# Kernel tuning notes

Measured on AMD Instinct MI355X. Metric: run time of the kernel, lower is better.

The kernel has to match this reference:

```python
import jax, jax.numpy as jnp
import numpy as np

N = 50000      # nodes
E = 800000     # edges (avg degree 16)
NF = 128       # input feature dim
H = 128        # hidden dim
GAMMA = 1.0    # gm init arg
COS_EPS = 1e-8 # F.cosine_similarity eps
EW_MIN = 1e-4  # edge-weight clamp


def setup_inputs() -> dict:
    key = jax.random.key(0)
    ks = jax.random.split(key, 9)
    x = jax.random.normal(ks[0], (N, NF), dtype=jnp.float32)
    edge_index = jax.random.randint(ks[1], (2, E), 0, N, dtype=jnp.int64)
    sensitive_attr = jax.random.randint(ks[2], (N,), 0, 2, dtype=jnp.int64)
    s1 = 1.0 / np.sqrt(NF)
    s2 = 1.0 / np.sqrt(H)
    W1 = jax.random.normal(ks[3], (NF, H), dtype=jnp.float32) * s1
    b1 = jnp.zeros((H,), dtype=jnp.float32)
    W2 = jax.random.normal(ks[4], (H, H), dtype=jnp.float32) * s2
    b2 = jnp.zeros((H,), dtype=jnp.float32)
    Wc = jax.random.normal(ks[5], (H, 1), dtype=jnp.float32) * s2
    bc = jnp.zeros((1,), dtype=jnp.float32)
    return {"x": x, "edge_index": edge_index, "sensitive_attr": sensitive_attr,
            "W1": W1, "b1": b1, "W2": W2, "b2": b2, "Wc": Wc, "bc": bc}


def gcn_conv(x, W, b, src, dst, ew, n):
    """PyG GCNConv: lin -> symmetric-normalized edge-weighted aggregation (+self loops) -> bias."""
    xt = x @ W                                              # [N,H]
    deg = jax.ops.segment_sum(ew, dst, num_segments=n) + 1.0  # self-loop weight 1
    dinv = jnp.where(deg > 0, deg ** -0.5, 0.0)             # [N]
    norm = dinv[src] * ew * dinv[dst]                       # [E]
    agg = jax.ops.segment_sum(xt[src] * norm[:, None], dst, num_segments=n)
    # self-loop contribution: norm_ii = dinv[i] * 1 * dinv[i]
    return agg + xt * (dinv * dinv)[:, None] + b


def reference(x, edge_index, sensitive_attr, W1, b1, W2, b2, Wc, bc):
    src, dst = edge_index[0], edge_index[1]
    # cosine-similarity edge weights (gather-heavy)
    xs, xd = x[src], x[dst]                                  # [E,F] each
    dot = jnp.sum(xs * xd, axis=1)
    ns = jnp.maximum(jnp.sqrt(jnp.sum(xs * xs, axis=1)), COS_EPS)
    nd = jnp.maximum(jnp.sqrt(jnp.sum(xd * xd, axis=1)), COS_EPS)
    sim = dot / (ns * nd)
    sen_diff = (sensitive_attr[src] != sensitive_attr[dst]).astype(x.dtype)
    ew = jnp.maximum(sim * jnp.exp(-GAMMA * sen_diff), EW_MIN)
    # two GCN layers (dropout is identity in eval mode)
    h = jax.nn.relu(gcn_conv(x, W1, b1, src, dst, ew, N))
    h = jax.nn.relu(gcn_conv(h, W2, b2, src, dst, ew, N))
    y = h @ Wc + bc                                          # [N,1]
    return (y, h)
```

## Files before the change

### kernel.cpp

```cpp
#include <hip/hip_runtime.h>


typedef unsigned short u16;
typedef unsigned int u32;
typedef __attribute__((ext_vector_type(8))) short short8;
typedef __attribute__((ext_vector_type(4))) float floatx4;

__device__ __forceinline__ float bflo(u32 u){ return __uint_as_float(u << 16); }
__device__ __forceinline__ float bfhi(u32 u){ return __uint_as_float(u & 0xFFFF0000u); }
__device__ __forceinline__ float bf1(u16 u){ return __uint_as_float(((u32)u) << 16); }
__device__ __forceinline__ u16 f2bf(float f){
    u32 u = __float_as_uint(f);
    u += 0x7FFFu + ((u >> 16) & 1u);
    return (u16)(u >> 16);
}
__device__ __forceinline__ u32 pack2(float a, float b){
    return (u32)f2bf(a) | ((u32)f2bf(b) << 16);
}
__device__ __forceinline__ float wsum(float v){
#pragma unroll
    for (int o = 32; o > 0; o >>= 1) v += __shfl_xor(v, o, 64);
    return v;
}
__device__ __forceinline__ float ld1(const void* p, size_t idx, int f32){
    return f32 ? ((const float*)p)[idx] : bf1(((const u16*)p)[idx]);
}
__device__ __forceinline__ int ldidx(const int* p, size_t i, int i64){
    return i64 ? p[2 * i] : p[i];
}

__global__ void classify_k(const u32* __restrict__ xw, const int* __restrict__ eiw,
                           int* __restrict__ flags, int* __restrict__ bcnt)
{
    __shared__ int c_out, c_nz;
    int t = threadIdx.x;
    if (t == 0) { c_out = 0; c_nz = 0; }
    if (t < 256) bcnt[t] = 0;
    __syncthreads();
    u32 w = xw[t];
    int e = (w >> 7) & 0xFF;
    int outl = (e < 110 || e > 140) ? 1 : 0;
    int nz = (eiw[2 * t + 1] != 0) ? 1 : 0;
    atomicAdd(&c_out, outl);
    atomicAdd(&c_nz, nz);
    __syncthreads();
    if (t == 0) { flags[0] = (c_out > 256); flags[1] = (c_nz < 256); }
}

__global__ __launch_bounds__(256) void convhist_k(const void* __restrict__ x,
                                                  u32* __restrict__ xb,
                                                  float* __restrict__ rn, int N,
                                                  const int* __restrict__ ei,
                                                  const int* __restrict__ sa,
                                                  int* __restrict__ bcnt, int E,
                                                  const void* __restrict__ W1,
                                                  const void* __restrict__ W2,
                                                  uint4* __restrict__ wf1,
                                                  uint4* __restrict__ wf2,
                                                  const int* __restrict__ flags,
                                                  int nbN, int nbH)
{
    __shared__ int lb[256];
    int b = blockIdx.x;
    if (b < nbN) {
        int i = b * 4 + (threadIdx.x >> 6);
        if (i >= N) return;
        int lane = threadIdx.x & 63;
        u32 u;
        if (flags[0]) {
            const float* q = (const float*)x + (size_t)i * 128 + lane * 2;
            u = pack2(q[0], q[1]);
        } else u = ((const u32*)x)[(size_t)i * 64 + lane];
        xb[(size_t)i * 64 + lane] = u;
        float f0 = bflo(u), f1 = bfhi(u);
        float ss = wsum(f0 * f0 + f1 * f1);
        if (lane == 0) {
            float r = 1.0f / fmaxf(sqrtf(ss), 1e-8f);
            int a = flags[1] ? sa[2 * (size_t)i] : sa[i];
            rn[i] = a ? -r : r;
        }
    } else if (b < nbN + nbH) {
        int t = threadIdx.x;
        lb[t] = 0;
        __syncthreads();
        int i64 = flags[1];
        size_t base = (size_t)(b - nbN) * 8192;
#pragma unroll 4
        for (int k = 0; k < 32; ++k) {
            size_t e = base + (size_t)k * 256 + t;
            if (e < (size_t)E) {
                int d = ldidx(ei, (size_t)E + e, i64);
                if ((u32)d >= (u32)N) d = 0;
                atomicAdd(&lb[d >> 8], 1);
            }
        }
        __syncthreads();
        int c = lb[t];
        if (c) atomicAdd(&bcnt[t], c);
    } else {
        int slot = (b - nbN - nbH) * 256 + threadIdx.x;
        if (slot >= 4096) return;
        int f32w = flags[0];
        const void* W = (slot < 2048) ? W1 : W2;
        uint4* wf = (slot < 2048) ? wf1 : wf2;
        int s = slot & 2047;
        int lane = s & 63, kk = (s >> 6) & 3, ct = s >> 8;
        int q = lane >> 4, n = lane & 15;
        int col = ct * 16 + n, k0 = kk * 32 + q * 8;
        union { u16 us[8]; uint4 u4; } tmp;
#pragma unroll
        for (int j = 0; j < 8; ++j)
            tmp.us[j] = f2bf(ld1(W, (size_t)(k0 + j) * 128 + col, f32w));
        wf[s] = tmp.u4;
    }
}

__global__ void bscan_k(const int* __restrict__ bcnt, int* __restrict__ bbase,
                        int* __restrict__ bcur, int* __restrict__ rowp, int N)
{
    int lane = threadIdx.x;
    int carry = 0;
    for (int base = 0; base < 256; base += 64) {
        int i = base + lane;
        int v = bcnt[i];
        int sc = v;
#pragma unroll
        for (int o = 1; o < 64; o <<= 1) {
            int nv = __shfl_up(sc, o);
            if (lane >= o) sc += nv;
        }
        int excl = carry + sc - v;
        bbase[i] = excl;
        bcur[i] = excl;
        carry += __shfl(sc, 63);
    }
    if (lane == 0) { bbase[256] = carry; rowp[N] = carry; }
}

__global__ __launch_bounds__(256) void bucket_k(const int* __restrict__ ei,
                                                int* __restrict__ bcur,
                                                u32* __restrict__ tmp,
                                                int E, int N,
                                                const int* __restrict__ flags)
{
    __shared__ int lh[256];
    __shared__ int gb[256];
    int t = threadIdx.x;
    lh[t] = 0;
    __syncthreads();
    int i64 = flags[1];
    size_t base = (size_t)blockIdx.x * 4096;
    u32 pay[16], meta[16];
#pragma unroll
    for (int k = 0; k < 16; ++k) {
        size_t e = base + (size_t)k * 256 + t;
        if (e < (size_t)E) {
            int s = ldidx(ei, e, i64);
            int d = ldidx(ei, (size_t)E + e, i64);
            if ((u32)s >= (u32)N) s = 0;
            if ((u32)d >= (u32)N) d = 0;
            int b = d >> 8;
            pay[k] = ((u32)s << 8) | ((u32)d & 0xFFu);
            int r = atomicAdd(&lh[b], 1);
            meta[k] = ((u32)r << 8) | (u32)b;
        } else meta[k] = 0xFFFFFFFFu;
    }
    __syncthreads();
    int c = lh[t];
    gb[t] = c ? atomicAdd(&bcur[t], c) : 0;
    __syncthreads();
#pragma unroll
    for (int k = 0; k < 16; ++k) {
        if (meta[k] != 0xFFFFFFFFu) {
            int b = (int)(meta[k] & 0xFFu);
            int r = (int)(meta[k] >> 8);
            tmp[gb[b] + r] = pay[k];
        }
    }
}

__global__ __launch_bounds__(256) void scat2_k(const int* __restrict__ bbase,
                                               int* __restrict__ rowp,
                                               const u32* __restrict__ tmp,
                                               u32* __restrict__ rec,
                                               int N, int E)
{
    __shared__ int lcnt[256];
    __shared__ int wtot[4];
    int b = blockIdx.x, t = threadIdx.x;
    int lane = t & 63, w = t >> 6;
    int n0 = b << 8;
    int p0 = bbase[b], p1 = bbase[b + 1];
    if (p0 < 0) p0 = 0;
    if (p1 > E) p1 = E;
    lcnt[t] = 0;
    __syncthreads();
    for (int idx = p0 + t; idx < p1; idx += 256)
        atomicAdd(&lcnt[tmp[idx] & 0xFFu], 1);
    __syncthreads();
    int v = lcnt[t];
    int sc = v;
#pragma unroll
    for (int o = 1; o < 64; o <<= 1) {
        int nv = __shfl_up(sc, o);
        if (lane >= o) sc += nv;
    }
    if (lane == 63) wtot[w] = sc;
    __syncthreads();
    int wo = 0;
#pragma unroll
    for (int k = 0; k < 4; ++k) { int s = wtot[k]; if (k < w) wo += s; }
    int excl = wo + sc - v;
    int node = n0 + t;
    if (node < N) rowp[node] = p0 + excl;
    lcnt[t] = excl;
    __syncthreads();
    for (int idx = p0 + t; idx < p1; idx += 256) {
        u32 pay = tmp[idx];
        int r = atomicAdd(&lcnt[pay & 0xFFu], 1);
        int pos = p0 + r;
        if ((u32)pos >= (u32)E) pos = 0;
        rec[pos] = pay >> 8;
    }
}

__global__ __launch_bounds__(256) void ewcsr_k(const u32* __restrict__ xb,
                                               const float* __restrict__ rn,
                                               const int* __restrict__ rowp,
                                               u32* __restrict__ rec,
                                               float* __restrict__ dv,
                                               int N, int E)
{
    int i = blockIdx.x * 4 + (threadIdx.x >> 6);
    if (i >= N) return;
    int lane = threadIdx.x & 63, g = lane >> 4, j = lane & 15;
    uint4 D = ((const uint4*)(xb + (size_t)i * 64))[j];
    float rni = rn[i];
    int p0 = rowp[i], p1 = rowp[i + 1];
    if (p0 < 0) p0 = 0;
    if (p1 > E) p1 = E;
    float acc = 0.0f;
    int p = p0 + g;
    for (; p + 4 < p1; p += 8) {
        int s0 = (int)rec[p];     if ((u32)s0 >= (u32)N) s0 = 0;
        int s1 = (int)rec[p + 4]; if ((u32)s1 >= (u32)N) s1 = 0;
        uint4 A0 = ((const uint4*)(xb + (size_t)s0 * 64))[j];
        uint4 A1 = ((const uint4*)(xb + (size_t)s1 * 64))[j];
        float d0 = bflo(A0.x) * bflo(D.x) + bfhi(A0.x) * bfhi(D.x)
                 + bflo(A0.y) * bflo(D.y) + bfhi(A0.y) * bfhi(D.y)
                 + bflo(A0.z) * bflo(D.z) + bfhi(A0.z) * bfhi(D.z)
                 + bflo(A0.w) * bflo(D.w) + bfhi(A0.w) * bfhi(D.w);
        float d1 = bflo(A1.x) * bflo(D.x) + bfhi(A1.x) * bfhi(D.x)
                 + bflo(A1.y) * bflo(D.y) + bfhi(A1.y) * bfhi(D.y)
                 + bflo(A1.z) * bflo(D.z) + bfhi(A1.z) * bfhi(D.z)
                 + bflo(A1.w) * bflo(D.w) + bfhi(A1.w) * bfhi(D.w);
#pragma unroll
        for (int o = 8; o > 0; o >>= 1) {
            d0 += __shfl_xor(d0, o);
            d1 += __shfl_xor(d1, o);
        }
        if (j == 0) {
            float pr0 = rn[s0] * rni;
            float w0 = fmaxf(d0 * fabsf(pr0) *
                             ((pr0 < 0.0f) ? 0.36787944117144233f : 1.0f), 1e-4f);
            u16 wb0 = f2bf(w0);
            rec[p] = ((u32)s0 << 16) | wb0;
            acc += bf1(wb0);
            float pr1 = rn[s1] * rni;
            float w1 = fmaxf(d1 * fabsf(pr1) *
                             ((pr1 < 0.0f) ? 0.36787944117144233f : 1.0f), 1e-4f);
            u16 wb1 = f2bf(w1);
            rec[p + 4] = ((u32)s1 << 16) | wb1;
            acc += bf1(wb1);
        }
    }
    if (p < p1) {
        int s0 = (int)rec[p]; if ((u32)s0 >= (u32)N) s0 = 0;
        uint4 A0 = ((const uint4*)(xb + (size_t)s0 * 64))[j];
        float d0 = bflo(A0.x) * bflo(D.x) + bfhi(A0.x) * bfhi(D.x)
                 + bflo(A0.y) * bflo(D.y) + bfhi(A0.y) * bfhi(D.y)
                 + bflo(A0.z) * bflo(D.z) + bfhi(A0.z) * bfhi(D.z)
                 + bflo(A0.w) * bflo(D.w) + bfhi(A0.w) * bfhi(D.w);
#pragma unroll
        for (int o = 8; o > 0; o >>= 1) d0 += __shfl_xor(d0, o);
        if (j == 0) {
            float pr0 = rn[s0] * rni;
            float w0 = fmaxf(d0 * fabsf(pr0) *
                             ((pr0 < 0.0f) ? 0.36787944117144233f : 1.0f), 1e-4f);
            u16 wb0 = f2bf(w0);
            rec[p] = ((u32)s0 << 16) | wb0;
            acc += bf1(wb0);
        }
    }
    acc += __shfl_xor(acc, 16);
    acc += __shfl_xor(acc, 32);
    if (lane == 0) dv[i] = 1.0f / sqrtf(1.0f + acc);
}

__global__ __launch_bounds__(256) void agg_k(const u32* __restrict__ feat,
                                             const int* __restrict__ rowp,
                                             const u32* __restrict__ rec,
                                             const float* __restrict__ dinv,
                                             u32* __restrict__ Tb, int N, int E)
{
    int i = blockIdx.x * 4 + (threadIdx.x >> 6);
    if (i >= N) return;
    int lane = threadIdx.x & 63;
    float di = dinv[i], sc = di * di;
    u32 u = feat[(size_t)i * 64 + lane];
    float a0 = bflo(u) * sc, a1 = bfhi(u) * sc;
    int p0 = rowp[i], p1 = rowp[i + 1];
    if (p0 < 0) p0 = 0;
    if (p1 > E) p1 = E;
    int p = p0;
    for (; p + 7 < p1; p += 8) {
        u32 r[8]; int s[8]; u32 v[8];
#pragma unroll
        for (int k = 0; k < 8; ++k) {
            r[k] = rec[p + k];
            s[k] = r[k] >> 16;
            if (s[k] >= N) s[k] = 0;
        }
#pragma unroll
        for (int k = 0; k < 8; ++k) v[k] = feat[(size_t)s[k] * 64 + lane];
#pragma unroll
        for (int k = 0; k < 8; ++k) {
            float w = bf1((u16)r[k]) * di * dinv[s[k]];
            a0 = fmaf(w, bflo(v[k]), a0);
            a1 = fmaf(w, bfhi(v[k]), a1);
        }
    }
    for (; p + 1 < p1; p += 2) {
        u32 r0 = rec[p], r1 = rec[p + 1];
        int s0 = r0 >> 16, s1 = r1 >> 16;
        if (s0 >= N) s0 = 0;
        if (s1 >= N) s1 = 0;
        u32 v0 = feat[(size_t)s0 * 64 + lane];
        u32 v1 = feat[(size_t)s1 * 64 + lane];
        float w0 = bf1((u16)r0) * di * dinv[s0];
        float w1 = bf1((u16)r1) * di * dinv[s1];
        a0 = fmaf(w0, bflo(v0), a0); a1 = fmaf(w0, bfhi(v0), a1);
        a0 = fmaf(w1, bflo(v1), a0); a1 = fmaf(w1, bfhi(v1), a1);
    }
    if (p < p1) {
        u32 r0 = rec[p];
        int s0 = r0 >> 16;
        if (s0 >= N) s0 = 0;
        u32 v0 = feat[(size_t)s0 * 64 + lane];
        float w0 = bf1((u16)r0) * di * dinv[s0];
        a0 = fmaf(w0, bflo(v0), a0); a1 = fmaf(w0, bfhi(v0), a1);
    }
    Tb[(size_t)i * 64 + lane] = pack2(a0, a1);
}

__global__ __launch_bounds__(256) void gemm_m(const u32* __restrict__ Tb,
                                              const uint4* __restrict__ wfrag,
                                              const void* __restrict__ bias,
                                              void* __restrict__ out, int outbf,
                                              int N,
                                              const void* __restrict__ Wc,
                                              const void* __restrict__ bc,
                                              float* __restrict__ yout,
                                              const int* __restrict__ flags)
{
    int t = threadIdx.x, wave = t >> 6, lane = t & 63;
    int q = lane >> 4, n = lane & 15;
    int f32w = flags[0];
    int rowbase = blockIdx.x * 64 + wave * 16;
    int arow = rowbase + n; if (arow > N - 1) arow = N - 1;
    const uint4* ap = (const uint4*)(Tb + (size_t)arow * 64);
    short8 a[4];
#pragma unroll
    for (int kk = 0; kk < 4; ++kk) {
        uint4 av = ap[kk * 4 + q];
        a[kk] = *(short8*)&av;
    }
    floatx4 acc[8];
#pragma unroll
    for (int ct = 0; ct < 8; ++ct) acc[ct] = (floatx4){0.f, 0.f, 0.f, 0.f};
#pragma unroll
    for (int ct = 0; ct < 8; ++ct) {
#pragma unroll
        for (int kk = 0; kk < 4; ++kk) {
            uint4 bv = wfrag[(ct * 4 + kk) * 64 + lane];
            acc[ct] = __builtin_amdgcn_mfma_f32_16x16x32_bf16(
                a[kk], *(short8*)&bv, acc[ct], 0, 0, 0);
        }
    }
    float bcv = 0.0f;
    float part[4] = {0.f, 0.f, 0.f, 0.f};
    if (yout) bcv = ld1(bc, 0, f32w);
#pragma unroll
    for (int ct = 0; ct < 8; ++ct) {
        int col = ct * 16 + n;
        float bia = ld1(bias, col, f32w);
        float wcv = yout ? ld1(Wc, col, f32w) : 0.0f;
#pragma unroll
        for (int r = 0; r < 4; ++r) {
            int row = rowbase + q * 4 + r;
            float h = fmaxf(acc[ct][r] + bia, 0.0f);
            if (row < N) {
                if (outbf) ((u16*)out)[(size_t)row * 128 + col] = f2bf(h);
                else       ((float*)out)[(size_t)row * 128 + col] = h;
            }
            part[r] = fmaf(h, wcv, part[r]);
        }
    }
    if (yout) {
#pragma unroll
        for (int r = 0; r < 4; ++r) {
            float pr = part[r];
#pragma unroll
            for (int o = 8; o > 0; o >>= 1) pr += __shfl_xor(pr, o);
            int row = rowbase + q * 4 + r;
            if (n == 0 && row < N) yout[row] = pr + bcv;
        }
    }
}

extern "C" void kernel_launch(void* const* d_in, const int* in_sizes, int n_in,
                              void* d_out, int out_size, void* d_ws, size_t ws_size,
                              hipStream_t stream)
{
    const void* x  = d_in[0];
    const int* ei  = (const int*)d_in[1];
    const int* sa  = (const int*)d_in[2];
    const void* W1 = d_in[3];
    const void* b1 = d_in[4];
    const void* W2 = d_in[5];
    const void* b2 = d_in[6];
    const void* Wc = d_in[7];
    const void* bc = d_in[8];
    const int N = in_sizes[2];
    const int E = in_sizes[1] / 2;

    float* y_out = (float*)d_out;
    float* h_out = y_out + N;
    u32*   Tbuf  = (u32*)d_in[0];
    u32*   tmp   = (u32*)d_in[0];

    const int nbN = (N + 3) / 4;
    const int nbH = (E + 8191) / 8192;
    const int NB  = (N + 255) / 256;

    char* p = (char*)d_ws;
    auto carve = [&](size_t bytes) { char* r = p; p += (bytes + 255) & ~(size_t)255; return r; };
    int*   flags = (int*)carve(256);
    float* rn    = (float*)carve((size_t)N * 4);
    float* dinv  = (float*)carve((size_t)N * 4);
    int*   rowp  = (int*)carve((size_t)(N + 1) * 4);
    int*   bcnt  = (int*)carve(256 * 4);
    int*   bbase = (int*)carve(260 * 4);
    int*   bcur  = (int*)carve(256 * 4);
    uint4* wf1   = (uint4*)carve(2048 * 16);
    uint4* wf2   = (uint4*)carve(2048 * 16);
    u32*   rec   = (u32*)carve((size_t)E * 4);
    u32*   xb    = (u32*)carve((size_t)N * 64 * 4);

    classify_k<<<1, 1024, 0, stream>>>((const u32*)x, ei, flags, bcnt);
    convhist_k<<<nbN + nbH + 16, 256, 0, stream>>>(x, xb, rn, N, ei, sa, bcnt, E,
                                                   W1, W2, wf1, wf2, flags,
                                                   nbN, nbH);
    bscan_k<<<1, 64, 0, stream>>>(bcnt, bbase, bcur, rowp, N);
    bucket_k<<<(E + 4095) / 4096, 256, 0, stream>>>(ei, bcur, tmp, E, N, flags);
    scat2_k<<<NB, 256, 0, stream>>>(bbase, rowp, tmp, rec, N, E);
    ewcsr_k<<<(N + 3) / 4, 256, 0, stream>>>(xb, rn, rowp, rec, dinv, N, E);

    agg_k<<<(N + 3) / 4, 256, 0, stream>>>(xb, rowp, rec, dinv, Tbuf, N, E);
    gemm_m<<<(N + 63) / 64, 256, 0, stream>>>(Tbuf, wf1, b1, xb, 1, N,
                                              nullptr, nullptr, nullptr, flags);
    agg_k<<<(N + 3) / 4, 256, 0, stream>>>(xb, rowp, rec, dinv, Tbuf, N, E);
    gemm_m<<<(N + 63) / 64, 256, 0, stream>>>(Tbuf, wf2, b2, h_out, 0, N,
                                              Wc, bc, y_out, flags);
}
```

Before: 276.0 us.

## Fuse neighbor aggregation with MFMA GEMM via shared-memory tile

Merges the aggregation kernel and the MFMA GEMM kernel into one kernel per layer. Each wave aggregates 16 rows into a padded LDS tile, then the block runs the bf16 MFMA GEMM directly from LDS, so the intermediate aggregated buffer never goes through global memory and two launches are dropped. In exchange, each wave now walks 16 rows one after another and the block count falls by 16x (about 782 blocks), which lowers the number of gathers in flight and the parallelism available to hide their latency. Layer 1 output is written into a separate buffer (the x input region) that layer 2 reads.

```diff
diff --git a/kernel.cpp b/kernel.cpp
--- a/kernel.cpp
+++ b/kernel.cpp
@@ -297,82 +297,81 @@
     if (lane == 0) dv[i] = 1.0f / sqrtf(1.0f + acc);
 }
 
-__global__ __launch_bounds__(256) void agg_k(const u32* __restrict__ feat,
-                                             const int* __restrict__ rowp,
-                                             const u32* __restrict__ rec,
-                                             const float* __restrict__ dinv,
-                                             u32* __restrict__ Tb, int N, int E)
-{
-    int i = blockIdx.x * 4 + (threadIdx.x >> 6);
-    if (i >= N) return;
-    int lane = threadIdx.x & 63;
-    float di = dinv[i], sc = di * di;
-    u32 u = feat[(size_t)i * 64 + lane];
-    float a0 = bflo(u) * sc, a1 = bfhi(u) * sc;
-    int p0 = rowp[i], p1 = rowp[i + 1];
-    if (p0 < 0) p0 = 0;
-    if (p1 > E) p1 = E;
-    int p = p0;
-    for (; p + 7 < p1; p += 8) {
-        u32 r[8]; int s[8]; u32 v[8];
-#pragma unroll
-        for (int k = 0; k < 8; ++k) {
-            r[k] = rec[p + k];
-            s[k] = r[k] >> 16;
-            if (s[k] >= N) s[k] = 0;
-        }
-#pragma unroll
-        for (int k = 0; k < 8; ++k) v[k] = feat[(size_t)s[k] * 64 + lane];
-#pragma unroll
-        for (int k = 0; k < 8; ++k) {
-            float w = bf1((u16)r[k]) * di * dinv[s[k]];
-            a0 = fmaf(w, bflo(v[k]), a0);
-            a1 = fmaf(w, bfhi(v[k]), a1);
-        }
-    }
-    for (; p + 1 < p1; p += 2) {
-        u32 r0 = rec[p], r1 = rec[p + 1];
-        int s0 = r0 >> 16, s1 = r1 >> 16;
-        if (s0 >= N) s0 = 0;
-        if (s1 >= N) s1 = 0;
-        u32 v0 = feat[(size_t)s0 * 64 + lane];
-        u32 v1 = feat[(size_t)s1 * 64 + lane];
-        float w0 = bf1((u16)r0) * di * dinv[s0];
-        float w1 = bf1((u16)r1) * di * dinv[s1];
-        a0 = fmaf(w0, bflo(v0), a0); a1 = fmaf(w0, bfhi(v0), a1);
-        a0 = fmaf(w1, bflo(v1), a0); a1 = fmaf(w1, bfhi(v1), a1);
-    }
-    if (p < p1) {
-        u32 r0 = rec[p];
-        int s0 = r0 >> 16;
-        if (s0 >= N) s0 = 0;
-        u32 v0 = feat[(size_t)s0 * 64 + lane];
-        float w0 = bf1((u16)r0) * di * dinv[s0];
-        a0 = fmaf(w0, bflo(v0), a0); a1 = fmaf(w0, bfhi(v0), a1);
-    }
-    Tb[(size_t)i * 64 + lane] = pack2(a0, a1);
-}
-
-__global__ __launch_bounds__(256) void gemm_m(const u32* __restrict__ Tb,
-                                              const uint4* __restrict__ wfrag,
-                                              const void* __restrict__ bias,
-                                              void* __restrict__ out, int outbf,
-                                              int N,
-                                              const void* __restrict__ Wc,
-                                              const void* __restrict__ bc,
-                                              float* __restrict__ yout,
-                                              const int* __restrict__ flags)
-{
+__global__ __launch_bounds__(256) void aggemm_k(const u32* __restrict__ feat,
+                                                const int* __restrict__ rowp,
+                                                const u32* __restrict__ rec,
+                                                const float* __restrict__ dinv,
+                                                const uint4* __restrict__ wfrag,
+                                                const void* __restrict__ bias,
+                                                void* __restrict__ out, int outbf,
+                                                int N, int E,
+                                                const void* __restrict__ Wc,
+                                                const void* __restrict__ bc,
+                                                float* __restrict__ yout,
+                                                const int* __restrict__ flags)
+{
+    __shared__ u32 T[64 * 68];
     int t = threadIdx.x, wave = t >> 6, lane = t & 63;
+    int rowbase = blockIdx.x * 64 + wave * 16;
+    for (int r = 0; r < 16; ++r) {
+        int i = rowbase + r;
+        float a0 = 0.0f, a1 = 0.0f;
+        if (i < N) {
+            float di = dinv[i], sc = di * di;
+            u32 u = feat[(size_t)i * 64 + lane];
+            a0 = bflo(u) * sc; a1 = bfhi(u) * sc;
+            int p0 = rowp[i], p1 = rowp[i + 1];
+            if (p0 < 0) p0 = 0;
+            if (p1 > E) p1 = E;
+            int p = p0;
+            for (; p + 7 < p1; p += 8) {
+                u32 rr[8]; int s[8]; u32 v[8];
+#pragma unroll
+                for (int k = 0; k < 8; ++k) {
+                    rr[k] = rec[p + k];
+                    s[k] = rr[k] >> 16;
+                    if (s[k] >= N) s[k] = 0;
+                }
+#pragma unroll
+                for (int k = 0; k < 8; ++k) v[k] = feat[(size_t)s[k] * 64 + lane];
+#pragma unroll
+                for (int k = 0; k < 8; ++k) {
+                    float w = bf1((u16)rr[k]) * di * dinv[s[k]];
+                    a0 = fmaf(w, bflo(v[k]), a0);
+                    a1 = fmaf(w, bfhi(v[k]), a1);
+                }
+            }
+            for (; p + 1 < p1; p += 2) {
+                u32 r0 = rec[p], r1 = rec[p + 1];
+                int s0 = r0 >> 16, s1 = r1 >> 16;
+                if (s0 >= N) s0 = 0;
+                if (s1 >= N) s1 = 0;
+                u32 v0 = feat[(size_t)s0 * 64 + lane];
+                u32 v1 = feat[(size_t)s1 * 64 + lane];
+                float w0 = bf1((u16)r0) * di * dinv[s0];
+                float w1 = bf1((u16)r1) * di * dinv[s1];
+                a0 = fmaf(w0, bflo(v0), a0); a1 = fmaf(w0, bfhi(v0), a1);
+                a0 = fmaf(w1, bflo(v1), a0); a1 = fmaf(w1, bfhi(v1), a1);
+            }
+            if (p < p1) {
+                u32 r0 = rec[p];
+                int s0 = r0 >> 16;
+                if (s0 >= N) s0 = 0;
+                u32 v0 = feat[(size_t)s0 * 64 + lane];
+                float w0 = bf1((u16)r0) * di * dinv[s0];
+                a0 = fmaf(w0, bflo(v0), a0); a1 = fmaf(w0, bfhi(v0), a1);
+            }
+        }
+        T[(wave * 16 + r) * 68 + lane] = pack2(a0, a1);
+    }
+    __syncthreads();
     int q = lane >> 4, n = lane & 15;
     int f32w = flags[0];
-    int rowbase = blockIdx.x * 64 + wave * 16;
-    int arow = rowbase + n; if (arow > N - 1) arow = N - 1;
-    const uint4* ap = (const uint4*)(Tb + (size_t)arow * 64);
+    const u32* ap = T + (size_t)(wave * 16 + n) * 68;
     short8 a[4];
 #pragma unroll
     for (int kk = 0; kk < 4; ++kk) {
-        uint4 av = ap[kk * 4 + q];
+        uint4 av = *(const uint4*)(ap + (kk * 4 + q) * 4);
         a[kk] = *(short8*)&av;
     }
     floatx4 acc[8];
@@ -436,7 +435,7 @@
 
     float* y_out = (float*)d_out;
     float* h_out = y_out + N;
-    u32*   Tbuf  = (u32*)d_in[0];
+    u32*   h1b   = (u32*)d_in[0];
     u32*   tmp   = (u32*)d_in[0];
 
     const int nbN = (N + 3) / 4;
@@ -466,10 +465,10 @@
     scat2_k<<<NB, 256, 0, stream>>>(bbase, rowp, tmp, rec, N, E);
     ewcsr_k<<<(N + 3) / 4, 256, 0, stream>>>(xb, rn, rowp, rec, dinv, N, E);
 
-    agg_k<<<(N + 3) / 4, 256, 0, stream>>>(xb, rowp, rec, dinv, Tbuf, N, E);
-    gemm_m<<<(N + 63) / 64, 256, 0, stream>>>(Tbuf, wf1, b1, xb, 1, N,
-                                              nullptr, nullptr, nullptr, flags);
-    agg_k<<<(N + 3) / 4, 256, 0, stream>>>(xb, rowp, rec, dinv, Tbuf, N, E);
-    gemm_m<<<(N + 63) / 64, 256, 0, stream>>>(Tbuf, wf2, b2, h_out, 0, N,
-                                              Wc, bc, y_out, flags);
-}
+    aggemm_k<<<(N + 63) / 64, 256, 0, stream>>>(xb, rowp, rec, dinv, wf1, b1,
+                                                h1b, 1, N, E,
+                                                nullptr, nullptr, nullptr, flags);
+    aggemm_k<<<(N + 63) / 64, 256, 0, stream>>>(h1b, rowp, rec, dinv, wf2, b2,
+                                                h_out, 0, N, E,
+                                                Wc, bc, y_out, flags);
+}
```

Measured after the change: 318.2 us. 15.3% more time.
